# Kernel tuning notes

Hardware: AMD Instinct MI355X
Metric: run time of the kernel (lower is better)

Reference implementation:

```python
import jax, jax.numpy as jnp
import numpy as np

N_PART = 60   # particles per jet (N)
P_FEAT = 30   # features per particle (P)
DE = 20       # edge latent dim
DO = 24       # node output dim
HID = 60      # MLP hidden width
NR = N_PART * (N_PART - 1)  # 3540 directed edges
BATCH = 2048

# receiver/sender indices in the same order as itertools.product with r != s
_pairs = np.array([(r, s) for r in range(N_PART) for s in range(N_PART) if r != s], dtype=np.int32)
R_IDX = jnp.asarray(_pairs[:, 0])  # [Nr] receiver node per edge
S_IDX = jnp.asarray(_pairs[:, 1])  # [Nr] sender node per edge


def _mlp(h, w1, b1, w2, b2, w3, b3):
    h = jax.nn.relu(h @ w1 + b1)
    h = jax.nn.relu(h @ w2 + b2)
    return jax.nn.relu(h @ w3 + b3)


def setup_inputs() -> dict:
    key = jax.random.key(0)
    ks = jax.random.split(key, 13)

    def w(k, shape):
        fan_in = shape[0]
        return jax.random.normal(k, shape, dtype=jnp.float32) * (1.0 / np.sqrt(fan_in))

    return {
        "x": jax.random.normal(ks[0], (BATCH, P_FEAT, N_PART), dtype=jnp.float32),
        # fr: 2P -> HID -> HID -> De
        "fr_w1": w(ks[1], (2 * P_FEAT, HID)), "fr_b1": jnp.zeros((HID,), jnp.float32),
        "fr_w2": w(ks[2], (HID, HID)),        "fr_b2": jnp.zeros((HID,), jnp.float32),
        "fr_w3": w(ks[3], (HID, DE)),         "fr_b3": jnp.zeros((DE,), jnp.float32),
        # fo: P+De -> HID -> HID -> Do
        "fo_w1": w(ks[4], (P_FEAT + DE, HID)), "fo_b1": jnp.zeros((HID,), jnp.float32),
        "fo_w2": w(ks[5], (HID, HID)),         "fo_b2": jnp.zeros((HID,), jnp.float32),
        "fo_w3": w(ks[6], (HID, DO)),          "fo_b3": jnp.zeros((DO,), jnp.float32),
    }


def reference(x, fr_w1, fr_b1, fr_w2, fr_b2, fr_w3, fr_b3,
              fo_w1, fo_b1, fo_w2, fo_b2, fo_w3, fo_b3):
    # x: [B, P, N]
    B = x.shape[0]
    # Gather receiver/sender node features per edge (equivalent to x @ Rr, x @ Rs)
    Orr = x[:, :, R_IDX]                      # [B, P, Nr]
    Ors = x[:, :, S_IDX]                      # [B, P, Nr]
    Bm = jnp.concatenate([Orr, Ors], axis=1)  # [B, 2P, Nr]
    Bm = jnp.swapaxes(Bm, 1, 2)               # [B, Nr, 2P]
    E = _mlp(Bm, fr_w1, fr_b1, fr_w2, fr_b2, fr_w3, fr_b3)  # [B, Nr, De]
    # Scatter-add edge messages back to receiver nodes (equivalent to einsum with Rr)
    Ebar = jnp.zeros((B, N_PART, DE), dtype=x.dtype).at[:, R_IDX].add(E)  # [B, N, De]
    # Node update
    C = jnp.concatenate([jnp.swapaxes(x, 1, 2), Ebar], axis=-1)  # [B, N, P+De]
    O = _mlp(C, fo_w1, fo_b1, fo_w2, fo_b2, fo_w3, fo_b3)        # [B, N, Do]
    return O.sum(axis=1)                                          # [B, Do]
```

## Files before the change

### kernel.cpp

```cpp
#include <hip/hip_runtime.h>

typedef _Float16 f16x8 __attribute__((ext_vector_type(8)));
typedef _Float16 f16x4 __attribute__((ext_vector_type(4)));
typedef float  f32x4  __attribute__((ext_vector_type(4)));
typedef unsigned int u32x4 __attribute__((ext_vector_type(4)));
typedef unsigned int u32x2 __attribute__((ext_vector_type(2)));

#define MFMA32F __builtin_amdgcn_mfma_f32_16x16x32_f16

__device__ __forceinline__ f32x4 mfma_k16(const f16x4& a, const f16x4& b, f32x4 c){
#if __has_builtin(__builtin_amdgcn_mfma_f32_16x16x16f16)
    return __builtin_amdgcn_mfma_f32_16x16x16f16(a, b, c, 0, 0, 0);
#else
    asm volatile("s_nop 1\n\t"
                 "v_mfma_f32_16x16x16_f16 %0, %1, %2, %0\n\t"
                 "s_nop 7\n\t"
                 "s_nop 7"
                 : "+v"(c)
                 : "v"(__builtin_bit_cast(u32x2, a)), "v"(__builtin_bit_cast(u32x2, b)));
    return c;
#endif
}

#define XT_S 0
#define A_S  2400
#define B_S  7008
#define EB_F 5808
#define O_F  7008
#define NSH  14064

__device__ __forceinline__ unsigned short hbits(float x){ return __builtin_bit_cast(unsigned short, (_Float16)x); }

__device__ __forceinline__ f16x8 addrelu16(u32x4 a, u32x4 b){
    f16x8 s = __builtin_bit_cast(f16x8, a) + __builtin_bit_cast(f16x8, b);
    const f16x8 z = {};
    return __builtin_elementwise_max(s, z);
}

__device__ __forceinline__ f16x4 relupack16(const f32x4& d){
    u32x2 u;
    u[0] = __builtin_bit_cast(unsigned int, __builtin_amdgcn_cvt_pkrtz(d[0], d[1]));
    u[1] = __builtin_bit_cast(unsigned int, __builtin_amdgcn_cvt_pkrtz(d[2], d[3]));
    const f16x4 z = {};
    return __builtin_elementwise_max(__builtin_bit_cast(f16x4, u), z);
}

__global__ __launch_bounds__(256, 3)
void innet_kernel(const float* __restrict__ x,
                  const float* __restrict__ fr_w1, const float* __restrict__ fr_b1,
                  const float* __restrict__ fr_w2, const float* __restrict__ fr_b2,
                  const float* __restrict__ fr_w3, const float* __restrict__ fr_b3,
                  const float* __restrict__ fo_w1, const float* __restrict__ fo_b1,
                  const float* __restrict__ fo_w2, const float* __restrict__ fo_b2,
                  const float* __restrict__ fo_w3, const float* __restrict__ fo_b3,
                  float* __restrict__ out)
{
    __shared__ __align__(16) unsigned short ss[NSH];
    float* sf = (float*)ss;

    const int b      = blockIdx.x;
    const int tid    = threadIdx.x;
    const int lane15 = tid & 15;
    const int g4     = (tid >> 4) & 3;
    const int w      = tid >> 6;

    const float* xb = x + b * 1800;
    for (int i = tid; i < 1800; i += 256){
        const int f = i / 60, p = i - f * 60;
        ss[XT_S + p * 40 + f] = hbits(xb[i]);
    }
    for (int i = tid; i < 600; i += 256){
        const int p = i / 10;
        ss[XT_S + p * 40 + 30 + (i - p * 10)] = 0;
    }
    for (int i = tid; i < 576; i += 256){
        const int arr = i / 288, rem = i - arr * 288;
        ss[(arr ? B_S : A_S) + 60 * 72 + rem] = 0;
    }
    for (int i = tid; i < 1200; i += 256) sf[EB_F + i] = 0.f;
    if (tid < 24) sf[O_F + tid] = 0.f;
    __syncthreads();

    {
        f16x8 w1af[4], w1bf[4];
        float b1v[4];
        #pragma unroll
        for (int n = 0; n < 4; ++n){
            const int col = n * 16 + lane15;
            const bool cvv = col < 60;
            b1v[n] = cvv ? fr_b1[col] : ((col == 60) ? 1.0f : 0.0f);
            #pragma unroll
            for (int j = 0; j < 8; ++j){
                const int f = g4 * 8 + j;
                w1af[n][j] = (_Float16)((f < 30 && cvv) ? fr_w1[f * 60 + col] : 0.f);
                w1bf[n][j] = (_Float16)((f < 30 && cvv) ? fr_w1[(30 + f) * 60 + col] : 0.f);
            }
        }
        const int pr_ = w * 16 + lane15;
        const u32x4 ux = *(const u32x4*)&ss[XT_S + pr_ * 40 + g4 * 8];
        const f16x8 xa = __builtin_bit_cast(f16x8, ux);
        const f32x4 z = {0.f, 0.f, 0.f, 0.f};
        f32x4 aA0 = MFMA32F(xa, w1af[0], z, 0, 0, 0);
        f32x4 aA1 = MFMA32F(xa, w1af[1], z, 0, 0, 0);
        f32x4 aA2 = MFMA32F(xa, w1af[2], z, 0, 0, 0);
        f32x4 aA3 = MFMA32F(xa, w1af[3], z, 0, 0, 0);
        f32x4 aB0 = MFMA32F(xa, w1bf[0], z, 0, 0, 0);
        f32x4 aB1 = MFMA32F(xa, w1bf[1], z, 0, 0, 0);
        f32x4 aB2 = MFMA32F(xa, w1bf[2], z, 0, 0, 0);
        f32x4 aB3 = MFMA32F(xa, w1bf[3], z, 0, 0, 0);
        #pragma unroll
        for (int reg = 0; reg < 4; ++reg){
            const int p = w * 16 + g4 * 4 + reg;
            if (p < 60){
                ss[A_S + p * 72 +      lane15] = hbits(aA0[reg] + b1v[0]);
                ss[A_S + p * 72 + 16 + lane15] = hbits(aA1[reg] + b1v[1]);
                ss[A_S + p * 72 + 32 + lane15] = hbits(aA2[reg] + b1v[2]);
                ss[A_S + p * 72 + 48 + lane15] = hbits(aA3[reg] + b1v[3]);
                ss[B_S + p * 72 +      lane15] = hbits(aB0[reg]);
                ss[B_S + p * 72 + 16 + lane15] = hbits(aB1[reg]);
                ss[B_S + p * 72 + 32 + lane15] = hbits(aB2[reg]);
                ss[B_S + p * 72 + 48 + lane15] = hbits(aB3[reg]);
            }
        }
    }
    __syncthreads();

    {
        f16x8 w2tf[4][2];
        #pragma unroll
        for (int m = 0; m < 4; ++m){
            const int row = m * 16 + lane15;
            #pragma unroll
            for (int c2 = 0; c2 < 2; ++c2){
                #pragma unroll
                for (int j = 0; j < 8; ++j){
                    const int k = c2 * 32 + g4 * 8 + j;
                    float v = 0.f;
                    if (row < 60)      v = (k < 60) ? fr_w2[k * 60 + row] : (k == 60 ? fr_b2[row] : 0.f);
                    else if (row == 60) v = (k == 60) ? 1.f : 0.f;
                    w2tf[m][c2][j] = (_Float16)v;
                }
            }
        }
        f16x4 w3tf[2][4];
        #pragma unroll
        for (int m2 = 0; m2 < 2; ++m2){
            const int e = m2 * 16 + lane15;
            #pragma unroll
            for (int c = 0; c < 4; ++c){
                #pragma unroll
                for (int j = 0; j < 4; ++j){
                    const int k = c * 16 + g4 * 4 + j;
                    float v = 0.f;
                    if (e < 20) v = (k < 60) ? fr_w3[k * 20 + e] : (k == 60 ? fr_b3[e] : 0.f);
                    w3tf[m2][c][j] = (_Float16)v;
                }
            }
        }

        #pragma unroll 1
        for (int r = w; r < 60; r += 4){
            const u32x4 a0 = *(const u32x4*)&ss[A_S + r * 72 + g4 * 8];
            const u32x4 a1 = *(const u32x4*)&ss[A_S + r * 72 + 32 + g4 * 8];
            f32x4 acc0 = {0.f,0.f,0.f,0.f}, acc1 = {0.f,0.f,0.f,0.f};
            #pragma unroll
            for (int st = 0; st < 4; ++st){
                const int s = st * 16 + lane15;
                const u32x4 bb0 = *(const u32x4*)&ss[B_S + s * 72 + g4 * 8];
                const u32x4 bb1 = *(const u32x4*)&ss[B_S + s * 72 + 32 + g4 * 8];
                const f16x8 h0 = addrelu16(a0, bb0);
                const f16x8 h1 = addrelu16(a1, bb1);
                f32x4 d0 = {0.f,0.f,0.f,0.f}, d1 = {0.f,0.f,0.f,0.f};
                f32x4 d2 = {0.f,0.f,0.f,0.f}, d3 = {0.f,0.f,0.f,0.f};
                d0 = MFMA32F(w2tf[0][0], h0, d0, 0,0,0); d0 = MFMA32F(w2tf[0][1], h1, d0, 0,0,0);
                d1 = MFMA32F(w2tf[1][0], h0, d1, 0,0,0); d1 = MFMA32F(w2tf[1][1], h1, d1, 0,0,0);
                d2 = MFMA32F(w2tf[2][0], h0, d2, 0,0,0); d2 = MFMA32F(w2tf[2][1], h1, d2, 0,0,0);
                d3 = MFMA32F(w2tf[3][0], h0, d3, 0,0,0); d3 = MFMA32F(w2tf[3][1], h1, d3, 0,0,0);
                const f16x4 hb0 = relupack16(d0), hb1 = relupack16(d1);
                const f16x4 hb2 = relupack16(d2), hb3 = relupack16(d3);
                f32x4 e0 = {0.f,0.f,0.f,0.f}, e1 = {0.f,0.f,0.f,0.f};
                e0 = mfma_k16(w3tf[0][0], hb0, e0); e0 = mfma_k16(w3tf[0][1], hb1, e0);
                e0 = mfma_k16(w3tf[0][2], hb2, e0); e0 = mfma_k16(w3tf[0][3], hb3, e0);
                e1 = mfma_k16(w3tf[1][0], hb0, e1); e1 = mfma_k16(w3tf[1][1], hb1, e1);
                e1 = mfma_k16(w3tf[1][2], hb2, e1); e1 = mfma_k16(w3tf[1][3], hb3, e1);
                const float vm = (s < 60 && s != r) ? 1.f : 0.f;
                #pragma unroll
                for (int reg = 0; reg < 4; ++reg){
                    acc0[reg] += vm * fmaxf(e0[reg], 0.f);
                    acc1[reg] += vm * fmaxf(e1[reg], 0.f);
                }
            }
            #pragma unroll
            for (int reg = 0; reg < 4; ++reg){
                float v0 = acc0[reg];
                v0 += __shfl_xor(v0, 1); v0 += __shfl_xor(v0, 2);
                v0 += __shfl_xor(v0, 4); v0 += __shfl_xor(v0, 8);
                float v1 = acc1[reg];
                v1 += __shfl_xor(v1, 1); v1 += __shfl_xor(v1, 2);
                v1 += __shfl_xor(v1, 4); v1 += __shfl_xor(v1, 8);
                if (lane15 == 0){
                    sf[EB_F + r * 20 + g4 * 4 + reg] += v0;
                    const int e1i = 16 + g4 * 4 + reg;
                    if (e1i < 20) sf[EB_F + r * 20 + e1i] += v1;
                }
            }
        }
    }
    __syncthreads();

    {
        const int p5 = w * 16 + lane15;
        const int pe = (p5 < 60) ? p5 : 0;
        const u32x4 uc0 = *(const u32x4*)&ss[XT_S + pe * 40 + g4 * 8];
        f16x8 cb0 = __builtin_bit_cast(f16x8, uc0);
        if (g4 == 3){
            cb0[6] = (_Float16)sf[EB_F + pe * 20 + 0];
            cb0[7] = (_Float16)sf[EB_F + pe * 20 + 1];
        }
        f16x8 cb1;
        #pragma unroll
        for (int j = 0; j < 8; ++j){
            const int k = 32 + g4 * 8 + j;
            float v;
            if (k < 50) v = sf[EB_F + pe * 20 + (k - 30)];
            else        v = (k == 50) ? 1.f : 0.f;
            cb1[j] = (_Float16)v;
        }
        f16x8 w1of[4][2];
        #pragma unroll
        for (int m = 0; m < 4; ++m){
            const int h = m * 16 + lane15;
            #pragma unroll
            for (int c2 = 0; c2 < 2; ++c2){
                #pragma unroll
                for (int j = 0; j < 8; ++j){
                    const int k = c2 * 32 + g4 * 8 + j;
                    float v = 0.f;
                    if (h < 60)      v = (k < 50) ? fo_w1[k * 60 + h] : (k == 50 ? fo_b1[h] : 0.f);
                    else if (h == 60) v = (k == 50) ? 1.f : 0.f;
                    w1of[m][c2][j] = (_Float16)v;
                }
            }
        }
        f32x4 d0 = {0.f,0.f,0.f,0.f}, d1 = {0.f,0.f,0.f,0.f};
        f32x4 d2 = {0.f,0.f,0.f,0.f}, d3 = {0.f,0.f,0.f,0.f};
        d0 = MFMA32F(w1of[0][0], cb0, d0, 0,0,0); d0 = MFMA32F(w1of[0][1], cb1, d0, 0,0,0);
        d1 = MFMA32F(w1of[1][0], cb0, d1, 0,0,0); d1 = MFMA32F(w1of[1][1], cb1, d1, 0,0,0);
        d2 = MFMA32F(w1of[2][0], cb0, d2, 0,0,0); d2 = MFMA32F(w1of[2][1], cb1, d2, 0,0,0);
        d3 = MFMA32F(w1of[3][0], cb0, d3, 0,0,0); d3 = MFMA32F(w1of[3][1], cb1, d3, 0,0,0);
        const f16x4 hb0 = relupack16(d0), hb1 = relupack16(d1);
        const f16x4 hb2 = relupack16(d2), hb3 = relupack16(d3);
        __builtin_amdgcn_sched_barrier(0);
        f16x4 w2of[4][4];
        #pragma unroll
        for (int m = 0; m < 4; ++m){
            const int h2 = m * 16 + lane15;
            #pragma unroll
            for (int c = 0; c < 4; ++c){
                #pragma unroll
                for (int j = 0; j < 4; ++j){
                    const int k = c * 16 + g4 * 4 + j;
                    float v = 0.f;
                    if (h2 < 60)      v = (k < 60) ? fo_w2[k * 60 + h2] : (k == 60 ? fo_b2[h2] : 0.f);
                    else if (h2 == 60) v = (k == 60) ? 1.f : 0.f;
                    w2of[m][c][j] = (_Float16)v;
                }
            }
        }
        f32x4 g0 = {0.f,0.f,0.f,0.f}, g1 = {0.f,0.f,0.f,0.f};
        f32x4 g2 = {0.f,0.f,0.f,0.f}, g3 = {0.f,0.f,0.f,0.f};
        g0 = mfma_k16(w2of[0][0], hb0, g0); g0 = mfma_k16(w2of[0][1], hb1, g0);
        g0 = mfma_k16(w2of[0][2], hb2, g0); g0 = mfma_k16(w2of[0][3], hb3, g0);
        g1 = mfma_k16(w2of[1][0], hb0, g1); g1 = mfma_k16(w2of[1][1], hb1, g1);
        g1 = mfma_k16(w2of[1][2], hb2, g1); g1 = mfma_k16(w2of[1][3], hb3, g1);
        g2 = mfma_k16(w2of[2][0], hb0, g2); g2 = mfma_k16(w2of[2][1], hb1, g2);
        g2 = mfma_k16(w2of[2][2], hb2, g2); g2 = mfma_k16(w2of[2][3], hb3, g2);
        g3 = mfma_k16(w2of[3][0], hb0, g3); g3 = mfma_k16(w2of[3][1], hb1, g3);
        g3 = mfma_k16(w2of[3][2], hb2, g3); g3 = mfma_k16(w2of[3][3], hb3, g3);
        const f16x4 gb0 = relupack16(g0), gb1 = relupack16(g1);
        const f16x4 gb2 = relupack16(g2), gb3 = relupack16(g3);
        __builtin_amdgcn_sched_barrier(0);
        f16x4 w3of[2][4];
        #pragma unroll
        for (int m2 = 0; m2 < 2; ++m2){
            const int o = m2 * 16 + lane15;
            #pragma unroll
            for (int c = 0; c < 4; ++c){
                #pragma unroll
                for (int j = 0; j < 4; ++j){
                    const int k = c * 16 + g4 * 4 + j;
                    float v = 0.f;
                    if (o < 24) v = (k < 60) ? fo_w3[k * 24 + o] : (k == 60 ? fo_b3[o] : 0.f);
                    w3of[m2][c][j] = (_Float16)v;
                }
            }
        }
        f32x4 o0 = {0.f,0.f,0.f,0.f}, o1 = {0.f,0.f,0.f,0.f};
        o0 = mfma_k16(w3of[0][0], gb0, o0); o0 = mfma_k16(w3of[0][1], gb1, o0);
        o0 = mfma_k16(w3of[0][2], gb2, o0); o0 = mfma_k16(w3of[0][3], gb3, o0);
        o1 = mfma_k16(w3of[1][0], gb0, o1); o1 = mfma_k16(w3of[1][1], gb1, o1);
        o1 = mfma_k16(w3of[1][2], gb2, o1); o1 = mfma_k16(w3of[1][3], gb3, o1);
        const float vm = (p5 < 60) ? 1.f : 0.f;
        #pragma unroll
        for (int reg = 0; reg < 4; ++reg){
            float v0 = vm * fmaxf(o0[reg], 0.f);
            v0 += __shfl_xor(v0, 1); v0 += __shfl_xor(v0, 2);
            v0 += __shfl_xor(v0, 4); v0 += __shfl_xor(v0, 8);
            float v1 = vm * fmaxf(o1[reg], 0.f);
            v1 += __shfl_xor(v1, 1); v1 += __shfl_xor(v1, 2);
            v1 += __shfl_xor(v1, 4); v1 += __shfl_xor(v1, 8);
            if (lane15 == 0){
                atomicAdd(&sf[O_F + g4 * 4 + reg], v0);
                const int oi = 16 + g4 * 4 + reg;
                if (oi < 24) atomicAdd(&sf[O_F + oi], v1);
            }
        }
    }
    __syncthreads();
    if (tid < 24) out[(size_t)b * 24 + tid] = sf[O_F + tid];
}

extern "C" void kernel_launch(void* const* d_in, const int* in_sizes, int n_in,
                              void* d_out, int out_size, void* d_ws, size_t ws_size,
                              hipStream_t stream) {
    const float* x      = (const float*)d_in[0];
    const float* fr_w1  = (const float*)d_in[1];
    const float* fr_b1  = (const float*)d_in[2];
    const float* fr_w2  = (const float*)d_in[3];
    const float* fr_b2  = (const float*)d_in[4];
    const float* fr_w3  = (const float*)d_in[5];
    const float* fr_b3  = (const float*)d_in[6];
    const float* fo_w1  = (const float*)d_in[7];
    const float* fo_b1  = (const float*)d_in[8];
    const float* fo_w2  = (const float*)d_in[9];
    const float* fo_b2  = (const float*)d_in[10];
    const float* fo_w3  = (const float*)d_in[11];
    const float* fo_b3  = (const float*)d_in[12];
    float* out = (float*)d_out;

    const int B = in_sizes[0] / 1800;
    innet_kernel<<<dim3(B), dim3(256), 0, stream>>>(
        x, fr_w1, fr_b1, fr_w2, fr_b2, fr_w3, fr_b3,
        fo_w1, fo_b1, fo_w2, fo_b2, fo_w3, fo_b3, out);
}
```

Before: 159.8 us.

## Prepack MLP weights into MFMA fragment layout in a prep kernel

Adds a single-block prep kernel that converts all weight and bias matrices to fp16 in the per-lane MFMA fragment layout and stores them in workspace. The main kernel then loads each fragment with one vector load instead of many scattered scalar loads with branches and conversions in every block. This removes redundant per-block weight gathering, at the cost of an extra small kernel launch that runs serially before the main kernel.

```diff
diff --git a/kernel.cpp b/kernel.cpp
--- a/kernel.cpp
+++ b/kernel.cpp
@@ -22,6 +22,15 @@
 #endif
 }
 
+#define OFF_W1AF 0
+#define OFF_W1BF 4096
+#define OFF_W2TF 8192
+#define OFF_W3TF 16384
+#define OFF_W1OF 20480
+#define OFF_W2OF 28672
+#define OFF_W3OF 36864
+#define OFF_B1V  40960
+
 #define XT_S 0
 #define A_S  2400
 #define B_S  7008
@@ -45,14 +54,90 @@
     return __builtin_elementwise_max(__builtin_bit_cast(f16x4, u), z);
 }
 
+__global__ void prep_kernel(const float* __restrict__ fr_w1, const float* __restrict__ fr_b1,
+                            const float* __restrict__ fr_w2, const float* __restrict__ fr_b2,
+                            const float* __restrict__ fr_w3, const float* __restrict__ fr_b3,
+                            const float* __restrict__ fo_w1, const float* __restrict__ fo_b1,
+                            const float* __restrict__ fo_w2, const float* __restrict__ fo_b2,
+                            const float* __restrict__ fo_w3, const float* __restrict__ fo_b3,
+                            void* __restrict__ wsv)
+{
+    const int l = threadIdx.x;
+    if (l >= 64) return;
+    const int lane15 = l & 15, g4 = (l >> 4) & 3;
+    unsigned short* ws = (unsigned short*)wsv;
+
+    for (int n = 0; n < 4; ++n){
+        const int col = n * 16 + lane15;
+        const bool cvv = col < 60;
+        for (int j = 0; j < 8; ++j){
+            const int f = g4 * 8 + j;
+            ws[OFF_W1AF/2 + (n*64+l)*8 + j] = hbits((f < 30 && cvv) ? fr_w1[f*60+col] : 0.f);
+            ws[OFF_W1BF/2 + (n*64+l)*8 + j] = hbits((f < 30 && cvv) ? fr_w1[(30+f)*60+col] : 0.f);
+        }
+    }
+    for (int m = 0; m < 4; ++m){
+        const int row = m * 16 + lane15;
+        for (int c2 = 0; c2 < 2; ++c2)
+            for (int j = 0; j < 8; ++j){
+                const int k = c2*32 + g4*8 + j;
+                float v = 0.f;
+                if (row < 60)       v = (k < 60) ? fr_w2[k*60+row] : (k == 60 ? fr_b2[row] : 0.f);
+                else if (row == 60) v = (k == 60) ? 1.f : 0.f;
+                ws[OFF_W2TF/2 + ((m*2+c2)*64+l)*8 + j] = hbits(v);
+            }
+    }
+    for (int m2 = 0; m2 < 2; ++m2){
+        const int e = m2 * 16 + lane15;
+        for (int c = 0; c < 4; ++c)
+            for (int j = 0; j < 4; ++j){
+                const int k = c*16 + g4*4 + j;
+                float v = 0.f;
+                if (e < 20) v = (k < 60) ? fr_w3[k*20+e] : (k == 60 ? fr_b3[e] : 0.f);
+                ws[OFF_W3TF/2 + ((m2*4+c)*64+l)*4 + j] = hbits(v);
+            }
+    }
+    for (int m = 0; m < 4; ++m){
+        const int h = m * 16 + lane15;
+        for (int c2 = 0; c2 < 2; ++c2)
+            for (int j = 0; j < 8; ++j){
+                const int k = c2*32 + g4*8 + j;
+                float v = 0.f;
+                if (h < 60)       v = (k < 50) ? fo_w1[k*60+h] : (k == 50 ? fo_b1[h] : 0.f);
+                else if (h == 60) v = (k == 50) ? 1.f : 0.f;
+                ws[OFF_W1OF/2 + ((m*2+c2)*64+l)*8 + j] = hbits(v);
+            }
+    }
+    for (int m = 0; m < 4; ++m){
+        const int h2 = m * 16 + lane15;
+        for (int c = 0; c < 4; ++c)
+            for (int j = 0; j < 4; ++j){
+                const int k = c*16 + g4*4 + j;
+                float v = 0.f;
+                if (h2 < 60)       v = (k < 60) ? fo_w2[k*60+h2] : (k == 60 ? fo_b2[h2] : 0.f);
+                else if (h2 == 60) v = (k == 60) ? 1.f : 0.f;
+                ws[OFF_W2OF/2 + ((m*4+c)*64+l)*4 + j] = hbits(v);
+            }
+    }
+    for (int m2 = 0; m2 < 2; ++m2){
+        const int o = m2 * 16 + lane15;
+        for (int c = 0; c < 4; ++c)
+            for (int j = 0; j < 4; ++j){
+                const int k = c*16 + g4*4 + j;
+                float v = 0.f;
+                if (o < 24) v = (k < 60) ? fo_w3[k*24+o] : (k == 60 ? fo_b3[o] : 0.f);
+                ws[OFF_W3OF/2 + ((m2*4+c)*64+l)*4 + j] = hbits(v);
+            }
+    }
+    float* wb = (float*)((char*)wsv + OFF_B1V);
+    for (int n = 0; n < 4; ++n){
+        const int col = n * 16 + lane15;
+        wb[l*4 + n] = (col < 60) ? fr_b1[col] : ((col == 60) ? 1.0f : 0.0f);
+    }
+}
+
 __global__ __launch_bounds__(256, 3)
-void innet_kernel(const float* __restrict__ x,
-                  const float* __restrict__ fr_w1, const float* __restrict__ fr_b1,
-                  const float* __restrict__ fr_w2, const float* __restrict__ fr_b2,
-                  const float* __restrict__ fr_w3, const float* __restrict__ fr_b3,
-                  const float* __restrict__ fo_w1, const float* __restrict__ fo_b1,
-                  const float* __restrict__ fo_w2, const float* __restrict__ fo_b2,
-                  const float* __restrict__ fo_w3, const float* __restrict__ fo_b3,
+void innet_kernel(const float* __restrict__ x, const void* __restrict__ wsv,
                   float* __restrict__ out)
 {
     __shared__ __align__(16) unsigned short ss[NSH];
@@ -63,6 +148,8 @@
     const int lane15 = tid & 15;
     const int g4     = (tid >> 4) & 3;
     const int w      = tid >> 6;
+    const int l64    = tid & 63;
+    const char* wsb  = (const char*)wsv;
 
     const float* xb = x + b * 1800;
     for (int i = tid; i < 1800; i += 256){
@@ -83,19 +170,12 @@
 
     {
         f16x8 w1af[4], w1bf[4];
-        float b1v[4];
         #pragma unroll
         for (int n = 0; n < 4; ++n){
-            const int col = n * 16 + lane15;
-            const bool cvv = col < 60;
-            b1v[n] = cvv ? fr_b1[col] : ((col == 60) ? 1.0f : 0.0f);
-            #pragma unroll
-            for (int j = 0; j < 8; ++j){
-                const int f = g4 * 8 + j;
-                w1af[n][j] = (_Float16)((f < 30 && cvv) ? fr_w1[f * 60 + col] : 0.f);
-                w1bf[n][j] = (_Float16)((f < 30 && cvv) ? fr_w1[(30 + f) * 60 + col] : 0.f);
-            }
-        }
+            w1af[n] = *(const f16x8*)(wsb + OFF_W1AF + (n*64 + l64)*16);
+            w1bf[n] = *(const f16x8*)(wsb + OFF_W1BF + (n*64 + l64)*16);
+        }
+        const f32x4 b1v = *(const f32x4*)(wsb + OFF_B1V + l64*16);
         const int pr_ = w * 16 + lane15;
         const u32x4 ux = *(const u32x4*)&ss[XT_S + pr_ * 40 + g4 * 8];
         const f16x8 xa = __builtin_bit_cast(f16x8, ux);
@@ -128,35 +208,16 @@
     {
         f16x8 w2tf[4][2];
         #pragma unroll
-        for (int m = 0; m < 4; ++m){
-            const int row = m * 16 + lane15;
-            #pragma unroll
-            for (int c2 = 0; c2 < 2; ++c2){
-                #pragma unroll
-                for (int j = 0; j < 8; ++j){
-                    const int k = c2 * 32 + g4 * 8 + j;
-                    float v = 0.f;
-                    if (row < 60)      v = (k < 60) ? fr_w2[k * 60 + row] : (k == 60 ? fr_b2[row] : 0.f);
-                    else if (row == 60) v = (k == 60) ? 1.f : 0.f;
-                    w2tf[m][c2][j] = (_Float16)v;
-                }
-            }
-        }
+        for (int m = 0; m < 4; ++m)
+            #pragma unroll
+            for (int c2 = 0; c2 < 2; ++c2)
+                w2tf[m][c2] = *(const f16x8*)(wsb + OFF_W2TF + ((m*2+c2)*64 + l64)*16);
         f16x4 w3tf[2][4];
         #pragma unroll
-        for (int m2 = 0; m2 < 2; ++m2){
-            const int e = m2 * 16 + lane15;
-            #pragma unroll
-            for (int c = 0; c < 4; ++c){
-                #pragma unroll
-                for (int j = 0; j < 4; ++j){
-                    const int k = c * 16 + g4 * 4 + j;
-                    float v = 0.f;
-                    if (e < 20) v = (k < 60) ? fr_w3[k * 20 + e] : (k == 60 ? fr_b3[e] : 0.f);
-                    w3tf[m2][c][j] = (_Float16)v;
-                }
-            }
-        }
+        for (int m2 = 0; m2 < 2; ++m2)
+            #pragma unroll
+            for (int c = 0; c < 4; ++c)
+                w3tf[m2][c] = *(const f16x4*)(wsb + OFF_W3TF + ((m2*4+c)*64 + l64)*8);
 
         #pragma unroll 1
         for (int r = w; r < 60; r += 4){
@@ -228,20 +289,10 @@
         }
         f16x8 w1of[4][2];
         #pragma unroll
-        for (int m = 0; m < 4; ++m){
-            const int h = m * 16 + lane15;
-            #pragma unroll
-            for (int c2 = 0; c2 < 2; ++c2){
-                #pragma unroll
-                for (int j = 0; j < 8; ++j){
-                    const int k = c2 * 32 + g4 * 8 + j;
-                    float v = 0.f;
-                    if (h < 60)      v = (k < 50) ? fo_w1[k * 60 + h] : (k == 50 ? fo_b1[h] : 0.f);
-                    else if (h == 60) v = (k == 50) ? 1.f : 0.f;
-                    w1of[m][c2][j] = (_Float16)v;
-                }
-            }
-        }
+        for (int m = 0; m < 4; ++m)
+            #pragma unroll
+            for (int c2 = 0; c2 < 2; ++c2)
+                w1of[m][c2] = *(const f16x8*)(wsb + OFF_W1OF + ((m*2+c2)*64 + l64)*16);
         f32x4 d0 = {0.f,0.f,0.f,0.f}, d1 = {0.f,0.f,0.f,0.f};
         f32x4 d2 = {0.f,0.f,0.f,0.f}, d3 = {0.f,0.f,0.f,0.f};
         d0 = MFMA32F(w1of[0][0], cb0, d0, 0,0,0); d0 = MFMA32F(w1of[0][1], cb1, d0, 0,0,0);
@@ -253,20 +304,10 @@
         __builtin_amdgcn_sched_barrier(0);
         f16x4 w2of[4][4];
         #pragma unroll
-        for (int m = 0; m < 4; ++m){
-            const int h2 = m * 16 + lane15;
-            #pragma unroll
-            for (int c = 0; c < 4; ++c){
-                #pragma unroll
-                for (int j = 0; j < 4; ++j){
-                    const int k = c * 16 + g4 * 4 + j;
-                    float v = 0.f;
-                    if (h2 < 60)      v = (k < 60) ? fo_w2[k * 60 + h2] : (k == 60 ? fo_b2[h2] : 0.f);
-                    else if (h2 == 60) v = (k == 60) ? 1.f : 0.f;
-                    w2of[m][c][j] = (_Float16)v;
-                }
-            }
-        }
+        for (int m = 0; m < 4; ++m)
+            #pragma unroll
+            for (int c = 0; c < 4; ++c)
+                w2of[m][c] = *(const f16x4*)(wsb + OFF_W2OF + ((m*4+c)*64 + l64)*8);
         f32x4 g0 = {0.f,0.f,0.f,0.f}, g1 = {0.f,0.f,0.f,0.f};
         f32x4 g2 = {0.f,0.f,0.f,0.f}, g3 = {0.f,0.f,0.f,0.f};
         g0 = mfma_k16(w2of[0][0], hb0, g0); g0 = mfma_k16(w2of[0][1], hb1, g0);
@@ -282,19 +323,10 @@
         __builtin_amdgcn_sched_barrier(0);
         f16x4 w3of[2][4];
         #pragma unroll
-        for (int m2 = 0; m2 < 2; ++m2){
-            const int o = m2 * 16 + lane15;
-            #pragma unroll
-            for (int c = 0; c < 4; ++c){
-                #pragma unroll
-                for (int j = 0; j < 4; ++j){
-                    const int k = c * 16 + g4 * 4 + j;
-                    float v = 0.f;
-                    if (o < 24) v = (k < 60) ? fo_w3[k * 24 + o] : (k == 60 ? fo_b3[o] : 0.f);
-                    w3of[m2][c][j] = (_Float16)v;
-                }
-            }
-        }
+        for (int m2 = 0; m2 < 2; ++m2)
+            #pragma unroll
+            for (int c = 0; c < 4; ++c)
+                w3of[m2][c] = *(const f16x4*)(wsb + OFF_W3OF + ((m2*4+c)*64 + l64)*8);
         f32x4 o0 = {0.f,0.f,0.f,0.f}, o1 = {0.f,0.f,0.f,0.f};
         o0 = mfma_k16(w3of[0][0], gb0, o0); o0 = mfma_k16(w3of[0][1], gb1, o0);
         o0 = mfma_k16(w3of[0][2], gb2, o0); o0 = mfma_k16(w3of[0][3], gb3, o0);
@@ -338,8 +370,10 @@
     const float* fo_b3  = (const float*)d_in[12];
     float* out = (float*)d_out;
 
+    prep_kernel<<<dim3(1), dim3(64), 0, stream>>>(
+        fr_w1, fr_b1, fr_w2, fr_b2, fr_w3, fr_b3,
+        fo_w1, fo_b1, fo_w2, fo_b2, fo_w3, fo_b3, d_ws);
+
     const int B = in_sizes[0] / 1800;
-    innet_kernel<<<dim3(B), dim3(256), 0, stream>>>(
-        x, fr_w1, fr_b1, fr_w2, fr_b2, fr_w3, fr_b3,
-        fo_w1, fo_b1, fo_w2, fo_b2, fo_w3, fo_b3, out);
-}
+    innet_kernel<<<dim3(B), dim3(256), 0, stream>>>(x, d_ws, out);
+}
```

Result: faster. 150.3 us (-5.9%).
